# Kernel optimization log

Measured on AMD Instinct MI355X. Metric: run time of the kernel, lower is better.

## Reference

```python
import jax, jax.numpy as jnp
import numpy as np


def setup_inputs() -> dict:
    key = jax.random.key(0)
    k1, k2, k3, k4, k5, k6 = jax.random.split(key, 6)
    B, N, C, H = 4096, 64, 192, 6
    NW = 64  # windows per image; must divide B
    TABLE = 225  # (2*8-1)**2
    qkv = jax.random.normal(k1, (B, N, 3 * C), dtype=jnp.float32)
    rpi = jax.random.randint(k2, (N, N), 0, TABLE, dtype=jnp.int64)
    mask = jax.random.normal(k3, (NW, N, N), dtype=jnp.float32)
    rpb_table = jax.random.normal(k4, (TABLE, H), dtype=jnp.float32) * 0.02
    proj_w = jax.random.normal(k5, (C, C), dtype=jnp.float32) * 0.02
    proj_b = jax.random.normal(k6, (C,), dtype=jnp.float32) * 0.02
    return {"qkv": qkv, "rpi": rpi, "mask": mask, "rpb_table": rpb_table,
            "proj_w": proj_w, "proj_b": proj_b}


def reference(qkv, rpi, mask, rpb_table, proj_w, proj_b):
    b_, n, c3 = qkv.shape
    c = c3 // 3
    h = rpb_table.shape[1]           # num_heads
    hd = c // h                      # head_dim
    scale = hd ** (-0.5)
    # (b_, n, 3, h, hd) -> (3, b_, h, n, hd)
    qkv = qkv.reshape(b_, n, 3, h, hd).transpose(2, 0, 3, 1, 4)
    q, k, v = qkv[0] * scale, qkv[1], qkv[2]
    # windowed QK^T: [b_, h, n, n]
    attn = jnp.einsum('bhqd,bhkd->bhqk', q, k)
    # relative position bias gather: rpi [n,n] -> [h,n,n]
    bias = rpb_table[rpi].transpose(2, 0, 1)
    attn = attn + bias[None]
    # shift-window mask add
    nw = mask.shape[0]
    attn = attn.reshape(b_ // nw, nw, h, n, n) + mask[None, :, None]
    attn = attn.reshape(b_, h, n, n)
    attn = jax.nn.softmax(attn, axis=-1)
    # AV then output projection
    out = jnp.einsum('bhqk,bhkd->bhqd', attn, v)
    out = out.transpose(0, 2, 1, 3).reshape(b_, n, c)
    return out @ proj_w.T + proj_b
```

## Files before the change

kernel.cpp:

```cpp
#include <hip/hip_runtime.h>
#include <stdint.h>

typedef __bf16 bf16x8 __attribute__((ext_vector_type(8)));
typedef float f32x4 __attribute__((ext_vector_type(4)));

__device__ __forceinline__ unsigned short f2bf(float f) {
    union { float f; uint32_t u; } v; v.f = f;
    uint32_t u = v.u;
    return (unsigned short)((u + 0x7FFFu + ((u >> 16) & 1u)) >> 16);
}

#define QS_STRIDE 40
#define VT_STRIDE 72
#define PS_STRIDE 72
#define XS_STRIDE 200


__global__ void prep_bm(const int* __restrict__ rpi32,
                        const float* __restrict__ mask,
                        const float* __restrict__ rpb,
                        float* __restrict__ bm) {
    __shared__ int is64_s;
    int tid = threadIdx.x;
    if (tid == 0) {
        int s = 0;
        #pragma unroll
        for (int i = 0; i < 16; ++i) s |= rpi32[2 * i + 1];
        is64_s = (s == 0);
    }
    __syncthreads();
    int g = blockIdx.x * 256 + tid;
    int wh = g >> 12;
    int e  = g & 4095;
    int c = e >> 6, r = e & 63;
    int h = wh % 6, w = wh / 6;
    int rc = r * 64 + c;
    int rv = is64_s ? rpi32[2 * rc] : rpi32[rc];
    bm[g] = mask[w * 4096 + rc] + rpb[rv * 6 + h];
}

__global__ void prep_wf(const float* __restrict__ proj_w, unsigned short* __restrict__ wf) {
    int g = blockIdx.x * 256 + threadIdx.x;
    int e = g & 7;
    int lane = (g >> 3) & 63;
    int kkct = g >> 9;
    int kk = kkct / 12, ct = kkct % 12;
    int co = ct * 16 + (lane & 15);
    int ki = kk * 32 + (lane >> 4) * 8 + e;
    wf[g] = f2bf(proj_w[co * 192 + ki]);
}


__global__ __launch_bounds__(256, 4)
void winattn_fast(const float* __restrict__ qkv,
                  const float* __restrict__ bm,
                  const unsigned short* __restrict__ wf,
                  const float* __restrict__ proj_b,
                  float* __restrict__ out) {
    __shared__ __align__(16) unsigned short x_s[64 * XS_STRIDE];
    __shared__ __align__(16) unsigned short u_s[7424];

    unsigned short* q_s  = u_s;
    unsigned short* k_s  = u_s + 2560;
    unsigned short* vT_s = u_s + 5120;
    unsigned short* p_s  = u_s;

    const int tid  = threadIdx.x;
    const int b    = blockIdx.x;
    const int lane = tid & 63;
    const int wv   = tid >> 6;
    const int l16  = lane & 15;
    const int lhi  = lane >> 4;
    const int qbase = wv * 16;
    const float scale = 0.17677669529663687f;

    const float* qkv_b = qkv + (size_t)b * 64 * 576;
    const float* bm_w  = bm + (size_t)(b & 63) * 6 * 4096;

    for (int h = 0; h < 6; ++h) {
        if (h) __syncthreads();
        #pragma unroll
        for (int it = 0; it < 2; ++it) {
            int idx = tid + it * 256;
            int tok = idx >> 3, d = (idx & 7) << 2;
            const float4* base = (const float4*)(qkv_b + tok * 576 + h * 32 + d);
            float4 qv = base[0];
            float4 kv = base[48];
            float4 vv = base[96];
            ushort4 qh, kh;
            qh.x = f2bf(qv.x * scale); qh.y = f2bf(qv.y * scale);
            qh.z = f2bf(qv.z * scale); qh.w = f2bf(qv.w * scale);
            kh.x = f2bf(kv.x); kh.y = f2bf(kv.y); kh.z = f2bf(kv.z); kh.w = f2bf(kv.w);
            *(ushort4*)&q_s[tok * QS_STRIDE + d] = qh;
            *(ushort4*)&k_s[tok * QS_STRIDE + d] = kh;
            vT_s[(d + 0) * VT_STRIDE + tok] = f2bf(vv.x);
            vT_s[(d + 1) * VT_STRIDE + tok] = f2bf(vv.y);
            vT_s[(d + 2) * VT_STRIDE + tok] = f2bf(vv.z);
            vT_s[(d + 3) * VT_STRIDE + tok] = f2bf(vv.w);
        }
        __syncthreads();

        bf16x8 aq = *(const bf16x8*)&q_s[(qbase + l16) * QS_STRIDE + lhi * 8];
        float lg[4][4];
        #pragma unroll
        for (int nt = 0; nt < 4; ++nt) {
            bf16x8 bk = *(const bf16x8*)&k_s[(nt * 16 + l16) * QS_STRIDE + lhi * 8];
            f32x4 c = {0.f, 0.f, 0.f, 0.f};
            c = __builtin_amdgcn_mfma_f32_16x16x32_bf16(aq, bk, c, 0, 0, 0);
            #pragma unroll
            for (int j = 0; j < 4; ++j) lg[nt][j] = c[j];
        }
        const float* bmh = bm_w + h * 4096;
        #pragma unroll
        for (int nt = 0; nt < 4; ++nt) {
            float4 bv = *(const float4*)&bmh[(nt * 16 + l16) * 64 + qbase + lhi * 4];
            lg[nt][0] += bv.x; lg[nt][1] += bv.y; lg[nt][2] += bv.z; lg[nt][3] += bv.w;
        }
        float srow[4];
        float p[4][4];
        #pragma unroll
        for (int j = 0; j < 4; ++j) {
            float m = fmaxf(fmaxf(lg[0][j], lg[1][j]), fmaxf(lg[2][j], lg[3][j]));
            #pragma unroll
            for (int o = 1; o < 16; o <<= 1) m = fmaxf(m, __shfl_xor(m, o, 64));
            float s = 0.f;
            #pragma unroll
            for (int nt = 0; nt < 4; ++nt) { p[nt][j] = __expf(lg[nt][j] - m); s += p[nt][j]; }
            #pragma unroll
            for (int o = 1; o < 16; o <<= 1) s += __shfl_xor(s, o, 64);
            srow[j] = s;
        }
        __syncthreads();
        unsigned short* pw = p_s + wv * 16 * PS_STRIDE;
        #pragma unroll
        for (int nt = 0; nt < 4; ++nt)
            #pragma unroll
            for (int j = 0; j < 4; ++j)
                pw[(lhi * 4 + j) * PS_STRIDE + nt * 16 + l16] = f2bf(p[nt][j]);
        __syncthreads();

        f32x4 xo[2] = {{0.f,0.f,0.f,0.f},{0.f,0.f,0.f,0.f}};
        #pragma unroll
        for (int kk = 0; kk < 2; ++kk) {
            bf16x8 pa = *(const bf16x8*)&pw[l16 * PS_STRIDE + kk * 32 + lhi * 8];
            #pragma unroll
            for (int dt = 0; dt < 2; ++dt) {
                bf16x8 vb = *(const bf16x8*)&vT_s[(dt * 16 + l16) * VT_STRIDE + kk * 32 + lhi * 8];
                xo[dt] = __builtin_amdgcn_mfma_f32_16x16x32_bf16(pa, vb, xo[dt], 0, 0, 0);
            }
        }
        #pragma unroll
        for (int j = 0; j < 4; ++j) {
            float inv = __builtin_amdgcn_rcpf(srow[j]);
            int n = qbase + lhi * 4 + j;
            #pragma unroll
            for (int dt = 0; dt < 2; ++dt)
                x_s[n * XS_STRIDE + h * 32 + dt * 16 + l16] = f2bf(xo[dt][j] * inv);
        }
    }

    f32x4 oacc[12];
    #pragma unroll
    for (int ct = 0; ct < 12; ++ct) oacc[ct] = (f32x4){0.f, 0.f, 0.f, 0.f};
    #pragma unroll
    for (int kk = 0; kk < 6; ++kk) {
        bf16x8 ax = *(const bf16x8*)&x_s[(qbase + l16) * XS_STRIDE + kk * 32 + lhi * 8];
        #pragma unroll
        for (int ct = 0; ct < 12; ++ct) {
            bf16x8 bw = *(const bf16x8*)&wf[((kk * 12 + ct) * 64 + lane) * 8];
            oacc[ct] = __builtin_amdgcn_mfma_f32_16x16x32_bf16(ax, bw, oacc[ct], 0, 0, 0);
        }
    }
    float* outb = out + (size_t)b * 64 * 192;
    #pragma unroll
    for (int ct = 0; ct < 12; ++ct) {
        int co = ct * 16 + l16;
        float bias = proj_b[co];
        #pragma unroll
        for (int j = 0; j < 4; ++j) {
            int n = qbase + lhi * 4 + j;
            outb[n * 192 + co] = oacc[ct][j] + bias;
        }
    }
}


#define WS_STRIDE 40

__global__ __launch_bounds__(256)
void winattn_fused(const float* __restrict__ qkv,
                   const int* __restrict__ rpi32,
                   const float* __restrict__ mask,
                   const float* __restrict__ rpb_table,
                   const float* __restrict__ proj_w,
                   const float* __restrict__ proj_b,
                   float* __restrict__ out) {
    __shared__ __align__(16) unsigned short x_s[64 * XS_STRIDE];
    __shared__ __align__(16) unsigned short u_s[12032];
    __shared__ float rpb_s[225];
    __shared__ int rpi_is64_s;

    unsigned short* q_s  = u_s;
    unsigned short* k_s  = u_s + 2560;
    unsigned short* vT_s = u_s + 5120;
    unsigned short* p_s  = u_s + 7424;
    unsigned short* w_s  = u_s;

    const int tid  = threadIdx.x;
    const int b    = blockIdx.x;
    const int lane = tid & 63;
    const int wv   = tid >> 6;
    const int l16  = lane & 15;
    const int lhi  = lane >> 4;
    const int qbase = wv * 16;
    const float scale = 0.17677669529663687f;

    if (tid == 0) {
        int s = 0;
        #pragma unroll
        for (int i = 0; i < 16; ++i) s |= rpi32[2 * i + 1];
        rpi_is64_s = (s == 0) ? 1 : 0;
    }

    const float* maskw = mask + (size_t)(b & 63) * 4096;
    const float* qkv_b = qkv + (size_t)b * 64 * 576;

    for (int h = 0; h < 6; ++h) {
        for (int idx = tid; idx < 64 * 8; idx += 256) {
            int tok = idx >> 3, d = (idx & 7) << 2;
            const float4* base = (const float4*)(qkv_b + tok * 576 + h * 32 + d);
            float4 qv = base[0];
            float4 kv = base[48];
            float4 vv = base[96];
            ushort4 qh, kh;
            qh.x = f2bf(qv.x * scale); qh.y = f2bf(qv.y * scale);
            qh.z = f2bf(qv.z * scale); qh.w = f2bf(qv.w * scale);
            kh.x = f2bf(kv.x); kh.y = f2bf(kv.y); kh.z = f2bf(kv.z); kh.w = f2bf(kv.w);
            *(ushort4*)&q_s[tok * QS_STRIDE + d] = qh;
            *(ushort4*)&k_s[tok * QS_STRIDE + d] = kh;
            vT_s[(d + 0) * VT_STRIDE + tok] = f2bf(vv.x);
            vT_s[(d + 1) * VT_STRIDE + tok] = f2bf(vv.y);
            vT_s[(d + 2) * VT_STRIDE + tok] = f2bf(vv.z);
            vT_s[(d + 3) * VT_STRIDE + tok] = f2bf(vv.w);
        }
        if (tid < 225) rpb_s[tid] = rpb_table[tid * 6 + h];
        __syncthreads();
        const int is64 = rpi_is64_s;

        bf16x8 aq = *(const bf16x8*)&q_s[(qbase + l16) * QS_STRIDE + lhi * 8];
        float lg[4][4];
        #pragma unroll
        for (int nt = 0; nt < 4; ++nt) {
            bf16x8 bk = *(const bf16x8*)&k_s[(nt * 16 + l16) * QS_STRIDE + lhi * 8];
            f32x4 c = {0.f, 0.f, 0.f, 0.f};
            c = __builtin_amdgcn_mfma_f32_16x16x32_bf16(aq, bk, c, 0, 0, 0);
            #pragma unroll
            for (int j = 0; j < 4; ++j) lg[nt][j] = c[j];
        }
        #pragma unroll
        for (int nt = 0; nt < 4; ++nt) {
            int c = nt * 16 + l16;
            #pragma unroll
            for (int j = 0; j < 4; ++j) {
                int r = qbase + lhi * 4 + j;
                int e = r * 64 + c;
                int rv = is64 ? rpi32[2 * e] : rpi32[e];
                lg[nt][j] += rpb_s[rv] + maskw[e];
            }
        }
        float srow[4];
        float p[4][4];
        #pragma unroll
        for (int j = 0; j < 4; ++j) {
            float m = fmaxf(fmaxf(lg[0][j], lg[1][j]), fmaxf(lg[2][j], lg[3][j]));
            #pragma unroll
            for (int o = 1; o < 16; o <<= 1) m = fmaxf(m, __shfl_xor(m, o, 64));
            float s = 0.f;
            #pragma unroll
            for (int nt = 0; nt < 4; ++nt) { p[nt][j] = __expf(lg[nt][j] - m); s += p[nt][j]; }
            #pragma unroll
            for (int o = 1; o < 16; o <<= 1) s += __shfl_xor(s, o, 64);
            srow[j] = s;
        }
        unsigned short* pw = p_s + wv * 16 * PS_STRIDE;
        #pragma unroll
        for (int nt = 0; nt < 4; ++nt)
            #pragma unroll
            for (int j = 0; j < 4; ++j)
                pw[(lhi * 4 + j) * PS_STRIDE + nt * 16 + l16] = f2bf(p[nt][j]);
        __syncthreads();

        f32x4 xo[2] = {{0.f,0.f,0.f,0.f},{0.f,0.f,0.f,0.f}};
        #pragma unroll
        for (int kk = 0; kk < 2; ++kk) {
            bf16x8 pa = *(const bf16x8*)&pw[l16 * PS_STRIDE + kk * 32 + lhi * 8];
            #pragma unroll
            for (int dt = 0; dt < 2; ++dt) {
                bf16x8 vb = *(const bf16x8*)&vT_s[(dt * 16 + l16) * VT_STRIDE + kk * 32 + lhi * 8];
                xo[dt] = __builtin_amdgcn_mfma_f32_16x16x32_bf16(pa, vb, xo[dt], 0, 0, 0);
            }
        }
        #pragma unroll
        for (int j = 0; j < 4; ++j) {
            float inv = 1.f / srow[j];
            int n = qbase + lhi * 4 + j;
            #pragma unroll
            for (int dt = 0; dt < 2; ++dt)
                x_s[n * XS_STRIDE + h * 32 + dt * 16 + l16] = f2bf(xo[dt][j] * inv);
        }
        __syncthreads();
    }

    f32x4 oacc[12];
    #pragma unroll
    for (int ct = 0; ct < 12; ++ct) oacc[ct] = (f32x4){0.f, 0.f, 0.f, 0.f};
    for (int kk = 0; kk < 6; ++kk) {
        for (int idx = tid; idx < 192 * 8; idx += 256) {
            int co = idx >> 3, d = (idx & 7) << 2;
            float4 wvv = *(const float4*)(proj_w + co * 192 + kk * 32 + d);
            ushort4 wh;
            wh.x = f2bf(wvv.x); wh.y = f2bf(wvv.y); wh.z = f2bf(wvv.z); wh.w = f2bf(wvv.w);
            *(ushort4*)&w_s[co * WS_STRIDE + d] = wh;
        }
        __syncthreads();
        bf16x8 ax = *(const bf16x8*)&x_s[(qbase + l16) * XS_STRIDE + kk * 32 + lhi * 8];
        #pragma unroll
        for (int ct = 0; ct < 12; ++ct) {
            bf16x8 bw = *(const bf16x8*)&w_s[(ct * 16 + l16) * WS_STRIDE + lhi * 8];
            oacc[ct] = __builtin_amdgcn_mfma_f32_16x16x32_bf16(ax, bw, oacc[ct], 0, 0, 0);
        }
        __syncthreads();
    }
    float* outb = out + (size_t)b * 64 * 192;
    #pragma unroll
    for (int ct = 0; ct < 12; ++ct) {
        int co = ct * 16 + l16;
        float bias = proj_b[co];
        #pragma unroll
        for (int j = 0; j < 4; ++j) {
            int n = qbase + lhi * 4 + j;
            outb[n * 192 + co] = oacc[ct][j] + bias;
        }
    }
}

extern "C" void kernel_launch(void* const* d_in, const int* in_sizes, int n_in,
                              void* d_out, int out_size, void* d_ws, size_t ws_size,
                              hipStream_t stream) {
    (void)in_sizes; (void)n_in; (void)out_size;
    const float* qkv       = (const float*)d_in[0];
    const int*   rpi       = (const int*)d_in[1];
    const float* mask      = (const float*)d_in[2];
    const float* rpb_table = (const float*)d_in[3];
    const float* proj_w    = (const float*)d_in[4];
    const float* proj_b    = (const float*)d_in[5];
    float* out = (float*)d_out;

    const size_t BM_BYTES = (size_t)64 * 6 * 4096 * sizeof(float);
    const size_t WF_BYTES = (size_t)36864 * sizeof(unsigned short);

    if (ws_size >= BM_BYTES + WF_BYTES) {
        float* bm = (float*)d_ws;
        unsigned short* wfp = (unsigned short*)((char*)d_ws + BM_BYTES);
        prep_bm<<<6144, 256, 0, stream>>>(rpi, mask, rpb_table, bm);
        prep_wf<<<144, 256, 0, stream>>>(proj_w, wfp);
        winattn_fast<<<4096, 256, 0, stream>>>(qkv, bm, wfp, proj_b, out);
    } else {
        winattn_fused<<<4096, 256, 0, stream>>>(qkv, rpi, mask, rpb_table, proj_w, proj_b, out);
    }
}
```

Before: 222.0 us.

## Prefetch next head's QKV into registers, give P its own buffer, merge prep kernels

The attention kernel now loads the next head's q/k/v into registers while it computes the current head, and writes them to shared memory only after the head finishes. P gets a dedicated shared buffer, which removes two barriers per head. Launch bounds drop from 4 to 3 blocks per CU to make room for the extra registers and LDS. The two prep kernels are merged into a single launch, and a barrier is added in the fallback kernel.

```diff
diff --git a/kernel.cpp b/kernel.cpp
--- a/kernel.cpp
+++ b/kernel.cpp
@@ -15,43 +15,45 @@
 #define PS_STRIDE 72
 #define XS_STRIDE 200
 
-
-__global__ void prep_bm(const int* __restrict__ rpi32,
-                        const float* __restrict__ mask,
-                        const float* __restrict__ rpb,
-                        float* __restrict__ bm) {
-    __shared__ int is64_s;
+__global__ void prep_all(const int* __restrict__ rpi32,
+                         const float* __restrict__ mask,
+                         const float* __restrict__ rpb,
+                         const float* __restrict__ proj_w,
+                         float* __restrict__ bm,
+                         unsigned short* __restrict__ wf) {
+    int bid = blockIdx.x;
     int tid = threadIdx.x;
-    if (tid == 0) {
-        int s = 0;
-        #pragma unroll
-        for (int i = 0; i < 16; ++i) s |= rpi32[2 * i + 1];
-        is64_s = (s == 0);
-    }
-    __syncthreads();
-    int g = blockIdx.x * 256 + tid;
-    int wh = g >> 12;
-    int e  = g & 4095;
-    int c = e >> 6, r = e & 63;
-    int h = wh % 6, w = wh / 6;
-    int rc = r * 64 + c;
-    int rv = is64_s ? rpi32[2 * rc] : rpi32[rc];
-    bm[g] = mask[w * 4096 + rc] + rpb[rv * 6 + h];
-}
-
-__global__ void prep_wf(const float* __restrict__ proj_w, unsigned short* __restrict__ wf) {
-    int g = blockIdx.x * 256 + threadIdx.x;
-    int e = g & 7;
-    int lane = (g >> 3) & 63;
-    int kkct = g >> 9;
-    int kk = kkct / 12, ct = kkct % 12;
-    int co = ct * 16 + (lane & 15);
-    int ki = kk * 32 + (lane >> 4) * 8 + e;
-    wf[g] = f2bf(proj_w[co * 192 + ki]);
-}
-
-
-__global__ __launch_bounds__(256, 4)
+    if (bid < 6144) {
+        __shared__ int is64_s;
+        if (tid == 0) {
+            int s = 0;
+            #pragma unroll
+            for (int i = 0; i < 16; ++i) s |= rpi32[2 * i + 1];
+            is64_s = (s == 0);
+        }
+        __syncthreads();
+        int g = bid * 256 + tid;
+        int wh = g >> 12;
+        int e  = g & 4095;
+        int c = e >> 6, r = e & 63;
+        int h = wh % 6, w = wh / 6;
+        int rc = r * 64 + c;
+        int rv = is64_s ? rpi32[2 * rc] : rpi32[rc];
+        bm[g] = mask[w * 4096 + rc] + rpb[rv * 6 + h];
+    } else {
+        int g = (bid - 6144) * 256 + tid;
+        int e = g & 7;
+        int lane = (g >> 3) & 63;
+        int kkct = g >> 9;
+        int kk = kkct / 12, ct = kkct % 12;
+        int co = ct * 16 + (lane & 15);
+        int ki = kk * 32 + (lane >> 4) * 8 + e;
+        wf[g] = f2bf(proj_w[co * 192 + ki]);
+    }
+}
+
+
+__global__ __launch_bounds__(256, 3)
 void winattn_fast(const float* __restrict__ qkv,
                   const float* __restrict__ bm,
                   const unsigned short* __restrict__ wf,
@@ -59,11 +61,11 @@
                   float* __restrict__ out) {
     __shared__ __align__(16) unsigned short x_s[64 * XS_STRIDE];
     __shared__ __align__(16) unsigned short u_s[7424];
+    __shared__ __align__(16) unsigned short p_s[4 * 16 * PS_STRIDE];
 
     unsigned short* q_s  = u_s;
     unsigned short* k_s  = u_s + 2560;
     unsigned short* vT_s = u_s + 5120;
-    unsigned short* p_s  = u_s;
 
     const int tid  = threadIdx.x;
     const int b    = blockIdx.x;
@@ -77,28 +79,54 @@
     const float* qkv_b = qkv + (size_t)b * 64 * 576;
     const float* bm_w  = bm + (size_t)(b & 63) * 6 * 4096;
 
+    const int tokA = tid >> 3;
+    const int dA   = (tid & 7) << 2;
+    const float4* gA = (const float4*)(qkv_b + tokA * 576 + dA);
+    const float4* gB = (const float4*)(qkv_b + (tokA + 32) * 576 + dA);
+
+    float4 q0, k0, v0, q1, k1, v1;
+
+#define LOADH(h_)  do { int o = (h_) * 8;                         \
+        q0 = gA[o];      k0 = gA[o + 48]; v0 = gA[o + 96];        \
+        q1 = gB[o];      k1 = gB[o + 48]; v1 = gB[o + 96]; } while (0)
+
+#define STOREH() do {                                             \
+        ushort4 qh, kh;                                           \
+        qh.x = f2bf(q0.x * scale); qh.y = f2bf(q0.y * scale);     \
+        qh.z = f2bf(q0.z * scale); qh.w = f2bf(q0.w * scale);     \
+        kh.x = f2bf(k0.x); kh.y = f2bf(k0.y);                     \
+        kh.z = f2bf(k0.z); kh.w = f2bf(k0.w);                     \
+        *(ushort4*)&q_s[tokA * QS_STRIDE + dA] = qh;              \
+        *(ushort4*)&k_s[tokA * QS_STRIDE + dA] = kh;              \
+        vT_s[(dA + 0) * VT_STRIDE + tokA] = f2bf(v0.x);           \
+        vT_s[(dA + 1) * VT_STRIDE + tokA] = f2bf(v0.y);           \
+        vT_s[(dA + 2) * VT_STRIDE + tokA] = f2bf(v0.z);           \
+        vT_s[(dA + 3) * VT_STRIDE + tokA] = f2bf(v0.w);           \
+        qh.x = f2bf(q1.x * scale); qh.y = f2bf(q1.y * scale);     \
+        qh.z = f2bf(q1.z * scale); qh.w = f2bf(q1.w * scale);     \
+        kh.x = f2bf(k1.x); kh.y = f2bf(k1.y);                     \
+        kh.z = f2bf(k1.z); kh.w = f2bf(k1.w);                     \
+        *(ushort4*)&q_s[(tokA + 32) * QS_STRIDE + dA] = qh;       \
+        *(ushort4*)&k_s[(tokA + 32) * QS_STRIDE + dA] = kh;       \
+        vT_s[(dA + 0) * VT_STRIDE + tokA + 32] = f2bf(v1.x);      \
+        vT_s[(dA + 1) * VT_STRIDE + tokA + 32] = f2bf(v1.y);      \
+        vT_s[(dA + 2) * VT_STRIDE + tokA + 32] = f2bf(v1.z);      \
+        vT_s[(dA + 3) * VT_STRIDE + tokA + 32] = f2bf(v1.w); } while (0)
+
+    LOADH(0);
+    STOREH();
+
+    unsigned short* pw = p_s + wv * 16 * PS_STRIDE;
+
     for (int h = 0; h < 6; ++h) {
-        if (h) __syncthreads();
-        #pragma unroll
-        for (int it = 0; it < 2; ++it) {
-            int idx = tid + it * 256;
-            int tok = idx >> 3, d = (idx & 7) << 2;
-            const float4* base = (const float4*)(qkv_b + tok * 576 + h * 32 + d);
-            float4 qv = base[0];
-            float4 kv = base[48];
-            float4 vv = base[96];
-            ushort4 qh, kh;
-            qh.x = f2bf(qv.x * scale); qh.y = f2bf(qv.y * scale);
-            qh.z = f2bf(qv.z * scale); qh.w = f2bf(qv.w * scale);
-            kh.x = f2bf(kv.x); kh.y = f2bf(kv.y); kh.z = f2bf(kv.z); kh.w = f2bf(kv.w);
-            *(ushort4*)&q_s[tok * QS_STRIDE + d] = qh;
-            *(ushort4*)&k_s[tok * QS_STRIDE + d] = kh;
-            vT_s[(d + 0) * VT_STRIDE + tok] = f2bf(vv.x);
-            vT_s[(d + 1) * VT_STRIDE + tok] = f2bf(vv.y);
-            vT_s[(d + 2) * VT_STRIDE + tok] = f2bf(vv.z);
-            vT_s[(d + 3) * VT_STRIDE + tok] = f2bf(vv.w);
-        }
-        __syncthreads();
+        __syncthreads();
+        if (h < 5) LOADH(h + 1);
+
+        const float* bmh = bm_w + h * 4096;
+        float4 bv[4];
+        #pragma unroll
+        for (int nt = 0; nt < 4; ++nt)
+            bv[nt] = *(const float4*)&bmh[(nt * 16 + l16) * 64 + qbase + lhi * 4];
 
         bf16x8 aq = *(const bf16x8*)&q_s[(qbase + l16) * QS_STRIDE + lhi * 8];
         float lg[4][4];
@@ -107,15 +135,10 @@
             bf16x8 bk = *(const bf16x8*)&k_s[(nt * 16 + l16) * QS_STRIDE + lhi * 8];
             f32x4 c = {0.f, 0.f, 0.f, 0.f};
             c = __builtin_amdgcn_mfma_f32_16x16x32_bf16(aq, bk, c, 0, 0, 0);
-            #pragma unroll
-            for (int j = 0; j < 4; ++j) lg[nt][j] = c[j];
-        }
-        const float* bmh = bm_w + h * 4096;
-        #pragma unroll
-        for (int nt = 0; nt < 4; ++nt) {
-            float4 bv = *(const float4*)&bmh[(nt * 16 + l16) * 64 + qbase + lhi * 4];
-            lg[nt][0] += bv.x; lg[nt][1] += bv.y; lg[nt][2] += bv.z; lg[nt][3] += bv.w;
-        }
+            lg[nt][0] = c[0] + bv[nt].x; lg[nt][1] = c[1] + bv[nt].y;
+            lg[nt][2] = c[2] + bv[nt].z; lg[nt][3] = c[3] + bv[nt].w;
+        }
+
         float srow[4];
         float p[4][4];
         #pragma unroll
@@ -130,14 +153,12 @@
             for (int o = 1; o < 16; o <<= 1) s += __shfl_xor(s, o, 64);
             srow[j] = s;
         }
-        __syncthreads();
-        unsigned short* pw = p_s + wv * 16 * PS_STRIDE;
+
         #pragma unroll
         for (int nt = 0; nt < 4; ++nt)
             #pragma unroll
             for (int j = 0; j < 4; ++j)
                 pw[(lhi * 4 + j) * PS_STRIDE + nt * 16 + l16] = f2bf(p[nt][j]);
-        __syncthreads();
 
         f32x4 xo[2] = {{0.f,0.f,0.f,0.f},{0.f,0.f,0.f,0.f}};
         #pragma unroll
@@ -157,7 +178,12 @@
             for (int dt = 0; dt < 2; ++dt)
                 x_s[n * XS_STRIDE + h * 32 + dt * 16 + l16] = f2bf(xo[dt][j] * inv);
         }
-    }
+
+        __syncthreads();
+        if (h < 5) STOREH();
+    }
+#undef LOADH
+#undef STOREH
 
     f32x4 oacc[12];
     #pragma unroll
@@ -282,6 +308,7 @@
             for (int o = 1; o < 16; o <<= 1) s += __shfl_xor(s, o, 64);
             srow[j] = s;
         }
+        __syncthreads();
         unsigned short* pw = p_s + wv * 16 * PS_STRIDE;
         #pragma unroll
         for (int nt = 0; nt < 4; ++nt)
@@ -360,11 +387,10 @@
     const size_t WF_BYTES = (size_t)36864 * sizeof(unsigned short);
 
     if (ws_size >= BM_BYTES + WF_BYTES) {
-        float* bm = (float*)d_ws;
+        float* bmp = (float*)d_ws;
         unsigned short* wfp = (unsigned short*)((char*)d_ws + BM_BYTES);
-        prep_bm<<<6144, 256, 0, stream>>>(rpi, mask, rpb_table, bm);
-        prep_wf<<<144, 256, 0, stream>>>(proj_w, wfp);
-        winattn_fast<<<4096, 256, 0, stream>>>(qkv, bm, wfp, proj_b, out);
+        prep_all<<<6144 + 144, 256, 0, stream>>>(rpi, mask, rpb_table, proj_w, bmp, wfp);
+        winattn_fast<<<4096, 256, 0, stream>>>(qkv, bmp, wfp, proj_b, out);
     } else {
         winattn_fused<<<4096, 256, 0, stream>>>(qkv, rpi, mask, rpb_table, proj_w, proj_b, out);
     }
```

Measured after the change: 213.0 us. -4.0%, faster.
